# Kernel optimization log

Hardware: AMD Instinct MI355X
Metric: run time of the kernel (lower is better)

The kernel has to match this reference:

```python
import jax, jax.numpy as jnp
import numpy as np

N_SIGMA = 2
N_CLASS = 8
FG_WEIGHT = jnp.array([10., 10., 10., 40., 80., 100., 60., 20.], dtype=jnp.float32)
W_INST, W_VAR, W_SEED = 1.0, 10.0, 1.0
MIN_PIXELS = 128


def lovasz_hinge_flat(logits, labels):
    # logits, labels: [P] flat; labels in {0,1}
    signs = 2.0 * labels - 1.0
    errors = 1.0 - logits * signs
    order = jnp.argsort(-errors)  # descending
    errors_sorted = errors[order]
    gt_sorted = labels[order]
    gts = gt_sorted.sum()
    inter = gts - jnp.cumsum(gt_sorted)
    union = gts + jnp.cumsum(1.0 - gt_sorted)
    jac = 1.0 - inter / union
    grad = jnp.concatenate([jac[:1], jac[1:] - jac[:-1]])
    return jnp.dot(jax.nn.relu(errors_sorted), jax.lax.stop_gradient(grad))


def setup_inputs() -> dict:
    key = jax.random.key(0)
    k1, k2, k3, k4 = jax.random.split(key, 4)
    B, H, W, N = 2, 512, 1024, 8
    prediction = jax.random.normal(k1, (B, 12, H, W), dtype=jnp.float32)
    bbox = jax.random.randint(k2, (B, 9, H, W), 0, 2, dtype=jnp.int32)
    masks = jax.random.randint(k3, (B, N, H, W), 0, 2, dtype=jnp.int32)
    cls_ids = jax.random.randint(k4, (B, N), 0, 8, dtype=jnp.int32)
    return {"prediction": prediction, "bbox": bbox, "masks": masks, "cls_ids": cls_ids}


def _forward(prediction, bbox, masks, cls_ids):
    B, C, H, W = prediction.shape
    N = masks.shape[1]
    sg = jax.lax.stop_gradient
    # coordinate map: full 2048/1024 linspace sliced to [:W]/[:H], as in the buffer
    xm = jnp.linspace(0.0, 2.0, 2048, dtype=prediction.dtype)[:W]
    ym = jnp.linspace(0.0, 1.0, 1024, dtype=prediction.dtype)[:H]
    xym = jnp.stack([jnp.broadcast_to(xm[None, :], (H, W)),
                     jnp.broadcast_to(ym[:, None], (H, W))], axis=0)  # [2,H,W]

    spatial_emb = jnp.tanh(prediction[:, 0:2]) + xym[None]            # [B,2,H,W]
    sigma = prediction[:, 2:2 + N_SIGMA]                               # [B,2,H,W]
    seed = jax.nn.sigmoid(prediction[:, 2 + N_SIGMA:2 + N_SIGMA + N_CLASS])  # [B,8,H,W]

    # background seed loss: sum over cls 1..8 of seed[cls-1]^2 where bbox[cls]==0
    bg = bbox[:, 1:9] == 0                                             # [B,8,H,W]
    seed_bg = jnp.sum(jnp.where(bg, seed * seed, 0.0), axis=(1, 2, 3))  # [B]

    m = (masks > 0).astype(prediction.dtype)                           # [B,N,H,W]
    cnt = m.sum(axis=(2, 3))                                           # [B,N]
    valid = (cnt >= MIN_PIXELS).astype(prediction.dtype)               # [B,N]
    cnt_safe = jnp.maximum(cnt, 1.0)

    # per-instance masked means (to_center=False -> center from spatial_emb)
    center = jnp.einsum('bnhw,bchw->bnc', m, spatial_emb) / cnt_safe[..., None]  # [B,N,2]
    s_mean = jnp.einsum('bnhw,bchw->bnc', m, sigma) / cnt_safe[..., None]        # [B,N,2]

    # var loss: mean over [n_sigma, P] of (sigma_in - s.detach())^2
    diff2 = (sigma[:, None] - sg(s_mean)[..., None, None]) ** 2        # [B,N,2,H,W]
    var_inst = jnp.einsum('bnchw,bnhw->bn', diff2, m) / (N_SIGMA * cnt_safe)

    s_exp = jnp.exp(s_mean * 10.0)                                     # [B,N,2]
    d2 = (spatial_emb[:, None] - center[..., None, None]) ** 2         # [B,N,2,H,W]
    dist = jnp.exp(-jnp.einsum('bnchw,bnc->bnhw', d2, s_exp))          # [B,N,H,W]

    # lovasz hinge per instance on dist*2-1 vs mask
    logits = (dist * 2.0 - 1.0).reshape(B * N, H * W)
    labels = m.reshape(B * N, H * W)
    lov = jax.vmap(lovasz_hinge_flat)(logits, labels).reshape(B, N)    # [B,N]

    # foreground seed loss
    seed_cls = jnp.take_along_axis(seed, cls_ids[..., None, None].astype(jnp.int32), axis=1)  # [B,N,H,W]
    fw = FG_WEIGHT[cls_ids]                                            # [B,N]
    seed_fg = fw * jnp.einsum('bnhw,bnhw->bn', m, (seed_cls - sg(dist)) ** 2)

    obj = valid.sum(axis=1)                                            # [B]
    obj_safe = jnp.maximum(obj, 1.0)
    inst_l = jnp.sum(lov * valid, axis=1) / obj_safe
    var_l = jnp.sum(var_inst * valid, axis=1) / obj_safe
    seed_l = (seed_bg + jnp.sum(seed_fg * valid, axis=1)) / (H * W)
    loss = jnp.mean(W_INST * inst_l + W_VAR * var_l + W_SEED * seed_l)
    return loss


def reference(prediction, bbox, masks, cls_ids):
    return _forward(prediction, bbox, masks, cls_ids)
```

## Files before the change

### kernel.cpp

```cpp
#include <hip/hip_runtime.h>
#include <cstdint>
#include <cstddef>

#define HW 524288
#define HW4 131072
#define NBIN 1024


__device__ __forceinline__ float wred(float v) {
#pragma unroll
  for (int o = 32; o > 0; o >>= 1) v += __shfl_xor(v, o, 64);
  return v;
}

__device__ __forceinline__ float fsig(float x) {
  return __builtin_amdgcn_rcpf(1.f + __expf(-x));
}
__device__ __forceinline__ float ftanh(float x) {
  return 1.f - 2.f * __builtin_amdgcn_rcpf(__expf(2.f * x) + 1.f);
}

__global__ __launch_bounds__(256) void pass1(
    const float* __restrict__ pred, const int* __restrict__ masks,
    double* __restrict__ acc)
{
  const int b = blockIdx.y;
  const int tid = threadIdx.x;
  const float4* pb4 = (const float4*)(pred + (size_t)b * 12 * HW);
  const int4*   mk4 = (const int4*)(masks + (size_t)b * 8 * HW);

  float c[8] = {0}, cx[8] = {0}, cy[8] = {0}, sx[8] = {0}, sy[8] = {0},
        sxx[8] = {0}, syy[8] = {0};

#pragma unroll
  for (int k = 0; k < 2; k++) {
    const int g = blockIdx.x * 512 + k * 256 + tid;
    int idx = g << 2;
    int h = idx >> 10, w = idx & 1023;
    float4 p0 = pb4[g];
    float4 p1 = pb4[HW4 + g];
    float4 s0 = pb4[2 * HW4 + g];
    float4 s1 = pb4[3 * HW4 + g];
    int4 mv[8];
#pragma unroll
    for (int n = 0; n < 8; n++) mv[n] = mk4[n * HW4 + g];

    float p0v[4] = {p0.x, p0.y, p0.z, p0.w}, p1v[4] = {p1.x, p1.y, p1.z, p1.w};
    float s0v[4] = {s0.x, s0.y, s0.z, s0.w}, s1v[4] = {s1.x, s1.y, s1.z, s1.w};
    float exv[4], eyv[4];
#pragma unroll
    for (int j = 0; j < 4; j++) {
      exv[j] = ftanh(p0v[j]) + (float)((w + j) * (2.0 / 2047.0));
      eyv[j] = ftanh(p1v[j]) + (float)(h * (1.0 / 1023.0));
    }
#pragma unroll
    for (int n = 0; n < 8; n++) {
      int mvv[4] = {mv[n].x, mv[n].y, mv[n].z, mv[n].w};
#pragma unroll
      for (int j = 0; j < 4; j++) {
        float mf = (mvv[j] > 0) ? 1.f : 0.f;
        c[n] += mf; cx[n] += mf * exv[j]; cy[n] += mf * eyv[j];
        sx[n] += mf * s0v[j]; sy[n] += mf * s1v[j];
        sxx[n] += mf * s0v[j] * s0v[j]; syy[n] += mf * s1v[j] * s1v[j];
      }
    }
  }

  __shared__ float red[4][56];
  int lane = tid & 63, wid = tid >> 6;
#pragma unroll
  for (int n = 0; n < 8; n++) {
    float r0 = wred(c[n]),  r1 = wred(cx[n]), r2 = wred(cy[n]),
          r3 = wred(sx[n]), r4 = wred(sy[n]), r5 = wred(sxx[n]),
          r6 = wred(syy[n]);
    if (lane == 0) {
      red[wid][n * 7 + 0] = r0; red[wid][n * 7 + 1] = r1;
      red[wid][n * 7 + 2] = r2; red[wid][n * 7 + 3] = r3;
      red[wid][n * 7 + 4] = r4; red[wid][n * 7 + 5] = r5;
      red[wid][n * 7 + 6] = r6;
    }
  }
  __syncthreads();
  if (tid < 56) {
    float s = red[0][tid] + red[1][tid] + red[2][tid] + red[3][tid];
    int n = tid / 7, q = tid % 7;
    atomicAdd(&acc[((size_t)b * 8 + n) * 8 + q], (double)s);
  }
}

__global__ __launch_bounds__(1024) void pass3(
    const float* __restrict__ pred, const int* __restrict__ bbox,
    const int* __restrict__ masks, const int* __restrict__ cls_ids,
    double* __restrict__ acc, double* __restrict__ seedbg,
    unsigned long long* __restrict__ ghist)
{
  const int seg = blockIdx.y;
  const int b = seg >> 3, n = seg & 7;
  const int tid = threadIdx.x;
  __shared__ unsigned hist[NBIN];
  __shared__ float redf[16][2];
  for (int j = tid; j < NBIN; j += 1024) hist[j] = 0;

  const double* a = acc + seg * 8;
  double cntd = a[0];
  double cs = cntd < 1.0 ? 1.0 : cntd;
  float cxv = (float)(a[1] / cs), cyv = (float)(a[2] / cs);
  float sex = __expf((float)(a[3] / cs) * 10.f);
  float sey = __expf((float)(a[4] / cs) * 10.f);
  int cls = cls_ids[b * 8 + n];
  const float4* pb4 = (const float4*)(pred + (size_t)b * 12 * HW);
  const float4* sp4 = pb4 + (size_t)(4 + cls) * HW4;
  const float4* sb4 = pb4 + (size_t)(4 + n) * HW4;
  const int4*   mp4 = (const int4*)(masks + (size_t)seg * HW);
  const int4*   bb4 = (const int4*)(bbox + (size_t)b * 9 * HW) + (1 + n) * HW4;
  __syncthreads();

  float sf = 0.f, sbg = 0.f;
  int gbase = blockIdx.x * 4096;
#pragma unroll
  for (int i = 0; i < 4; i++) {
    int g = gbase + i * 1024 + tid;
    int idx = g << 2;
    int h = idx >> 10, w = idx & 1023;
    float4 p0 = pb4[g];
    float4 p1 = pb4[HW4 + g];
    int4 mv = mp4[g];
    float4 sv = sp4[g];
    float4 sb = sb4[g];
    int4 bv = bb4[g];
    float p0v[4] = {p0.x, p0.y, p0.z, p0.w}, p1v[4] = {p1.x, p1.y, p1.z, p1.w};
    float svv[4] = {sv.x, sv.y, sv.z, sv.w}, sbv[4] = {sb.x, sb.y, sb.z, sb.w};
    int mvv[4] = {mv.x, mv.y, mv.z, mv.w}, bvv[4] = {bv.x, bv.y, bv.z, bv.w};
#pragma unroll
    for (int j = 0; j < 4; j++) {
      int m = (mvv[j] > 0) ? 1 : 0;
      float ex = ftanh(p0v[j]) + (float)((w + j) * (2.0 / 2047.0));
      float ey = ftanh(p1v[j]) + (float)(h * (1.0 / 1023.0));
      float dx = ex - cxv, dy = ey - cyv;
      float d = __expf(-(dx * dx * sex + dy * dy * sey));
      float df = fsig(svv[j]) - d;
      sf += m ? df * df : 0.f;
      float sgb = fsig(sbv[j]);
      sbg += (bvv[j] == 0) ? sgb * sgb : 0.f;
      float e = m ? 2.f - 2.f * d : 2.f * d;
      int k = (int)(e * 512.f); k = k > (NBIN - 1) ? (NBIN - 1) : k;
      atomicAdd(&hist[k], m ? 65536u : 1u);
    }
  }
  __syncthreads();

  unsigned long long* gh = ghist + (size_t)seg * NBIN;
  for (int j = tid; j < NBIN; j += 1024) {
    unsigned v = hist[j];
    if (v)
      atomicAdd(&gh[j], (unsigned long long)(v & 0xffffu) |
                        ((unsigned long long)(v >> 16) << 32));
  }

  float r0 = wred(sf), r1 = wred(sbg);
  int lane = tid & 63, wid = tid >> 6;
  if (lane == 0) { redf[wid][0] = r0; redf[wid][1] = r1; }
  __syncthreads();
  if (tid == 0) {
    float t = 0.f;
    for (int w2 = 0; w2 < 16; w2++) t += redf[w2][0];
    atomicAdd(&acc[seg * 8 + 7], (double)t);
  } else if (tid == 64) {
    float t = 0.f;
    for (int w2 = 0; w2 < 16; w2++) t += redf[w2][1];
    atomicAdd(&seedbg[b], (double)t);
  }
}

__global__ __launch_bounds__(256) void pass4(
    const unsigned long long* __restrict__ ghist, const double* __restrict__ acc,
    const double* __restrict__ seedbg, const int* __restrict__ cls_ids,
    float* __restrict__ lov, unsigned* __restrict__ ctr,
    float* __restrict__ out)
{
  const int seg = blockIdx.x;
  const int tid = threadIdx.x;
  const int lane = tid & 63, wid = tid >> 6;
  __shared__ __align__(16) unsigned lh[NBIN * 2];
  __shared__ unsigned wc[4], wp[4];
  __shared__ double sred[4];

  const uint4* gh4 = (const uint4*)(ghist + (size_t)seg * NBIN);
#pragma unroll
  for (int i = 0; i < 2; i++)
    ((uint4*)lh)[i * 256 + tid] = gh4[i * 256 + tid];
  __syncthreads();

  double G = acc[seg * 8 + 0];

  unsigned cntT = 0, posT = 0;
#pragma unroll
  for (int i = 0; i < 4; i++) {
    int kk = (NBIN - 1) - tid * 4 - i;
    unsigned h0 = lh[2 * kk], h1 = lh[2 * kk + 1];
    cntT += h0 + h1; posT += h1;
  }
  unsigned ic = cntT, ip = posT;
  for (int o = 1; o < 64; o <<= 1) {
    unsigned yc = __shfl_up(ic, o, 64), yp = __shfl_up(ip, o, 64);
    if (lane >= o) { ic += yc; ip += yp; }
  }
  if (lane == 63) { wc[wid] = ic; wp[wid] = ip; }
  __syncthreads();
  unsigned oc = 0, op = 0;
  for (int w2 = 0; w2 < wid; w2++) { oc += wc[w2]; op += wp[w2]; }
  unsigned p = oc + ic - cntT, C = op + ip - posT;

  double S = 0.0;
#pragma unroll
  for (int i = 0; i < 4; i++) {
    int kk = (NBIN - 1) - tid * 4 - i;
    unsigned n1 = lh[2 * kk + 1], n0 = lh[2 * kk];
    double ec = (kk + 0.5) * (1.0 / 512.0);
    if (n1) {
      S += (double)n1 * ec / (G + (double)(p - C));
      p += n1; C += n1;
    }
    if (n0) {
      double rem = G - (double)C;
      if (rem > 0.0) {
        double aa = G + (double)(p - C);
        S += ec * rem * (1.0 / aa - 1.0 / (aa + (double)n0));
      }
      p += n0;
    }
  }
#pragma unroll
  for (int o = 32; o > 0; o >>= 1) S += __shfl_xor(S, o, 64);
  if (lane == 0) sred[wid] = S;
  __syncthreads();

  if (tid == 0) {
    double St = sred[0] + sred[1] + sred[2] + sred[3];
    atomicExch(&lov[seg], (float)St);
    __threadfence();
    unsigned old = atomicAdd(ctr, 1u);
    if (old == 15u) {
      __threadfence();
      const float FG[8] = {10.f, 10.f, 10.f, 40.f, 80.f, 100.f, 60.f, 20.f};
      double total = 0.0;
      for (int b = 0; b < 2; b++) {
        double obj = 0, inst = 0, varl = 0, sfg = 0;
        for (int n = 0; n < 8; n++) {
          int s = b * 8 + n;
          const double* a = acc + s * 8;
          double cnt = a[0];
          double cs = cnt < 1.0 ? 1.0 : cnt;
          double smx = a[3] / cs, smy = a[4] / cs;
          double var = ((a[5] - cnt * smx * smx) + (a[6] - cnt * smy * smy)) /
                       (2.0 * cs);
          double v = (cnt >= 128.0) ? 1.0 : 0.0;
          double lv = (double)atomicAdd(&lov[s], 0.0f);
          obj += v;
          inst += lv * v;
          varl += var * v;
          sfg += (double)FG[cls_ids[s]] * a[7] * v;
        }
        double objs = obj < 1.0 ? 1.0 : obj;
        double seedl = (seedbg[b] + sfg) / (double)HW;
        total += inst / objs + 10.0 * (varl / objs) + seedl;
      }
      out[0] = (float)(0.5 * total);
    }
  }
}

extern "C" void kernel_launch(void* const* d_in, const int* in_sizes, int n_in,
                              void* d_out, int out_size, void* d_ws, size_t ws_size,
                              hipStream_t stream)
{
  (void)in_sizes; (void)n_in; (void)out_size; (void)ws_size;
  const float* pred  = (const float*)d_in[0];
  const int*   bbox  = (const int*)d_in[1];
  const int*   masks = (const int*)d_in[2];
  const int*   cls   = (const int*)d_in[3];

  char* ws = (char*)d_ws;
  double*             acc    = (double*)(ws + 0);
  double*             seedbg = (double*)(ws + 1024);
  float*              lov    = (float*)(ws + 1040);
  unsigned*           ctr    = (unsigned*)(ws + 1104);
  unsigned long long* ghist  = (unsigned long long*)(ws + 4096);

  hipMemsetAsync(d_ws, 0, 135168, stream);
  pass1<<<dim3(256, 2), 256, 0, stream>>>(pred, masks, acc);
  pass3<<<dim3(32, 16), 1024, 0, stream>>>(pred, bbox, masks, cls, acc, seedbg, ghist);
  pass4<<<16, 256, 0, stream>>>(ghist, acc, seedbg, cls, lov, ctr, (float*)d_out);
}
```

Measured before the change: 170.9 us.

## Process all 8 instances per pixel block and dump per-block histograms

New measurement: 182.2 us. 1.07x slower.

```diff
diff --git a/kernel.cpp b/kernel.cpp
--- a/kernel.cpp
+++ b/kernel.cpp
@@ -88,87 +88,123 @@
   }
 }
 
-__global__ __launch_bounds__(1024) void pass3(
+__global__ __launch_bounds__(512) void pass3(
     const float* __restrict__ pred, const int* __restrict__ bbox,
     const int* __restrict__ masks, const int* __restrict__ cls_ids,
     double* __restrict__ acc, double* __restrict__ seedbg,
-    unsigned long long* __restrict__ ghist)
-{
-  const int seg = blockIdx.y;
+    unsigned* __restrict__ gdump)
+{
+  const int b = blockIdx.y;
+  const int tid = threadIdx.x;
+  __shared__ unsigned hist[8 * NBIN];
+  __shared__ float redf[8][9];
+
+  uint4* h4 = (uint4*)hist;
+  for (int j = tid; j < 2048; j += 512) h4[j] = make_uint4(0u, 0u, 0u, 0u);
+
+  float cxp[8], cyp[8], sexp[8], seyp[8];
+  int clsv[8];
+#pragma unroll
+  for (int n = 0; n < 8; n++) {
+    const double* a = acc + ((size_t)b * 8 + n) * 8;
+    double cs = a[0] < 1.0 ? 1.0 : a[0];
+    cxp[n] = (float)(a[1] / cs);
+    cyp[n] = (float)(a[2] / cs);
+    sexp[n] = __expf((float)(a[3] / cs) * 10.f);
+    seyp[n] = __expf((float)(a[4] / cs) * 10.f);
+    clsv[n] = cls_ids[b * 8 + n];
+  }
+  const float4* pb4 = (const float4*)(pred + (size_t)b * 12 * HW);
+  const int4*   mk4 = (const int4*)(masks + (size_t)b * 8 * HW);
+  const int4*   bb4 = (const int4*)(bbox + (size_t)b * 9 * HW);
+  __syncthreads();
+
+  const int g = blockIdx.x * 512 + tid;
+  const int idx = g << 2;
+  const int h = idx >> 10, w = idx & 1023;
+
+  float4 p0 = pb4[g];
+  float4 p1 = pb4[HW4 + g];
+  float ex[4], ey[4];
+  {
+    float p0v[4] = {p0.x, p0.y, p0.z, p0.w}, p1v[4] = {p1.x, p1.y, p1.z, p1.w};
+#pragma unroll
+    for (int j = 0; j < 4; j++) {
+      ex[j] = ftanh(p0v[j]) + (float)((w + j) * (2.0 / 2047.0));
+      ey[j] = ftanh(p1v[j]) + (float)(h * (1.0 / 1023.0));
+    }
+  }
+
+  float sbg = 0.f;
+  int lane = tid & 63, wid = tid >> 6;
+#pragma unroll
+  for (int n = 0; n < 8; n++) {
+    int4   mv = mk4[n * HW4 + g];
+    int4   bv = bb4[(1 + n) * HW4 + g];
+    float4 sc = pb4[(4 + clsv[n]) * HW4 + g];
+    float4 sb = pb4[(4 + n) * HW4 + g];
+    int mvv[4] = {mv.x, mv.y, mv.z, mv.w}, bvv[4] = {bv.x, bv.y, bv.z, bv.w};
+    float scv[4] = {sc.x, sc.y, sc.z, sc.w}, sbv[4] = {sb.x, sb.y, sb.z, sb.w};
+    float sf = 0.f;
+#pragma unroll
+    for (int j = 0; j < 4; j++) {
+      int m = (mvv[j] > 0) ? 1 : 0;
+      float dx = ex[j] - cxp[n], dy = ey[j] - cyp[n];
+      float d = __expf(-(dx * dx * sexp[n] + dy * dy * seyp[n]));
+      float df = fsig(scv[j]) - d;
+      sf += m ? df * df : 0.f;
+      float s0 = fsig(sbv[j]);
+      sbg += (bvv[j] == 0) ? s0 * s0 : 0.f;
+      float e = m ? 2.f - 2.f * d : 2.f * d;
+      int k = (int)(e * 512.f); k = k > (NBIN - 1) ? (NBIN - 1) : k;
+      atomicAdd(&hist[n * NBIN + k], m ? 65536u : 1u);
+    }
+    float r = wred(sf);
+    if (lane == 0) redf[wid][n] = r;
+  }
+  {
+    float r = wred(sbg);
+    if (lane == 0) redf[wid][8] = r;
+  }
+  __syncthreads();
+
+  uint4* dst = (uint4*)(gdump + ((size_t)(b * 256 + blockIdx.x) * 8) * NBIN);
+  for (int j = tid; j < 2048; j += 512) dst[j] = h4[j];
+
+  if (tid < 9) {
+    float t = 0.f;
+    for (int w2 = 0; w2 < 8; w2++) t += redf[w2][tid];
+    if (tid < 8)
+      atomicAdd(&acc[((size_t)b * 8 + tid) * 8 + 7], (double)t);
+    else
+      atomicAdd(&seedbg[b], (double)t);
+  }
+}
+
+__global__ __launch_bounds__(256) void pass4a(
+    const unsigned* __restrict__ gdump, unsigned long long* __restrict__ ghist)
+{
+  const int seg = blockIdx.x >> 4;
+  const int chunk = blockIdx.x & 15;
   const int b = seg >> 3, n = seg & 7;
   const int tid = threadIdx.x;
-  __shared__ unsigned hist[NBIN];
-  __shared__ float redf[16][2];
-  for (int j = tid; j < NBIN; j += 1024) hist[j] = 0;
-
-  const double* a = acc + seg * 8;
-  double cntd = a[0];
-  double cs = cntd < 1.0 ? 1.0 : cntd;
-  float cxv = (float)(a[1] / cs), cyv = (float)(a[2] / cs);
-  float sex = __expf((float)(a[3] / cs) * 10.f);
-  float sey = __expf((float)(a[4] / cs) * 10.f);
-  int cls = cls_ids[b * 8 + n];
-  const float4* pb4 = (const float4*)(pred + (size_t)b * 12 * HW);
-  const float4* sp4 = pb4 + (size_t)(4 + cls) * HW4;
-  const float4* sb4 = pb4 + (size_t)(4 + n) * HW4;
-  const int4*   mp4 = (const int4*)(masks + (size_t)seg * HW);
-  const int4*   bb4 = (const int4*)(bbox + (size_t)b * 9 * HW) + (1 + n) * HW4;
-  __syncthreads();
-
-  float sf = 0.f, sbg = 0.f;
-  int gbase = blockIdx.x * 4096;
+
+  unsigned neg[4] = {0, 0, 0, 0}, pos[4] = {0, 0, 0, 0};
+#pragma unroll
+  for (int xb = 0; xb < 16; xb++) {
+    int blk = chunk * 16 + xb;
+    const uint4 v = ((const uint4*)gdump)[(((size_t)b * 256 + blk) * 8 + n) * 256 + tid];
+    neg[0] += v.x & 0xffffu; pos[0] += v.x >> 16;
+    neg[1] += v.y & 0xffffu; pos[1] += v.y >> 16;
+    neg[2] += v.z & 0xffffu; pos[2] += v.z >> 16;
+    neg[3] += v.w & 0xffffu; pos[3] += v.w >> 16;
+  }
+  unsigned long long* gh = ghist + (size_t)seg * NBIN;
 #pragma unroll
   for (int i = 0; i < 4; i++) {
-    int g = gbase + i * 1024 + tid;
-    int idx = g << 2;
-    int h = idx >> 10, w = idx & 1023;
-    float4 p0 = pb4[g];
-    float4 p1 = pb4[HW4 + g];
-    int4 mv = mp4[g];
-    float4 sv = sp4[g];
-    float4 sb = sb4[g];
-    int4 bv = bb4[g];
-    float p0v[4] = {p0.x, p0.y, p0.z, p0.w}, p1v[4] = {p1.x, p1.y, p1.z, p1.w};
-    float svv[4] = {sv.x, sv.y, sv.z, sv.w}, sbv[4] = {sb.x, sb.y, sb.z, sb.w};
-    int mvv[4] = {mv.x, mv.y, mv.z, mv.w}, bvv[4] = {bv.x, bv.y, bv.z, bv.w};
-#pragma unroll
-    for (int j = 0; j < 4; j++) {
-      int m = (mvv[j] > 0) ? 1 : 0;
-      float ex = ftanh(p0v[j]) + (float)((w + j) * (2.0 / 2047.0));
-      float ey = ftanh(p1v[j]) + (float)(h * (1.0 / 1023.0));
-      float dx = ex - cxv, dy = ey - cyv;
-      float d = __expf(-(dx * dx * sex + dy * dy * sey));
-      float df = fsig(svv[j]) - d;
-      sf += m ? df * df : 0.f;
-      float sgb = fsig(sbv[j]);
-      sbg += (bvv[j] == 0) ? sgb * sgb : 0.f;
-      float e = m ? 2.f - 2.f * d : 2.f * d;
-      int k = (int)(e * 512.f); k = k > (NBIN - 1) ? (NBIN - 1) : k;
-      atomicAdd(&hist[k], m ? 65536u : 1u);
-    }
-  }
-  __syncthreads();
-
-  unsigned long long* gh = ghist + (size_t)seg * NBIN;
-  for (int j = tid; j < NBIN; j += 1024) {
-    unsigned v = hist[j];
-    if (v)
-      atomicAdd(&gh[j], (unsigned long long)(v & 0xffffu) |
-                        ((unsigned long long)(v >> 16) << 32));
-  }
-
-  float r0 = wred(sf), r1 = wred(sbg);
-  int lane = tid & 63, wid = tid >> 6;
-  if (lane == 0) { redf[wid][0] = r0; redf[wid][1] = r1; }
-  __syncthreads();
-  if (tid == 0) {
-    float t = 0.f;
-    for (int w2 = 0; w2 < 16; w2++) t += redf[w2][0];
-    atomicAdd(&acc[seg * 8 + 7], (double)t);
-  } else if (tid == 64) {
-    float t = 0.f;
-    for (int w2 = 0; w2 < 16; w2++) t += redf[w2][1];
-    atomicAdd(&seedbg[b], (double)t);
+    if (neg[i] | pos[i])
+      atomicAdd(&gh[tid * 4 + i],
+                (unsigned long long)neg[i] | ((unsigned long long)pos[i] << 32));
   }
 }
 
@@ -286,9 +322,11 @@
   float*              lov    = (float*)(ws + 1040);
   unsigned*           ctr    = (unsigned*)(ws + 1104);
   unsigned long long* ghist  = (unsigned long long*)(ws + 4096);
+  unsigned*           gdump  = (unsigned*)(ws + 262144);
 
   hipMemsetAsync(d_ws, 0, 135168, stream);
   pass1<<<dim3(256, 2), 256, 0, stream>>>(pred, masks, acc);
-  pass3<<<dim3(32, 16), 1024, 0, stream>>>(pred, bbox, masks, cls, acc, seedbg, ghist);
+  pass3<<<dim3(256, 2), 512, 0, stream>>>(pred, bbox, masks, cls, acc, seedbg, gdump);
+  pass4a<<<256, 256, 0, stream>>>(gdump, ghist);
   pass4<<<16, 256, 0, stream>>>(ghist, acc, seedbg, cls, lov, ctr, (float*)d_out);
 }
```

## Fuse Lovasz histogram scan into pass3 via last-block counter, split pass1 wider

Applied to the files above, without the earlier changes.

New measurement: 298.1 us. 74.4% more time.

```diff
diff --git a/kernel.cpp b/kernel.cpp
--- a/kernel.cpp
+++ b/kernel.cpp
@@ -12,7 +12,6 @@
   for (int o = 32; o > 0; o >>= 1) v += __shfl_xor(v, o, 64);
   return v;
 }
-
 __device__ __forceinline__ float fsig(float x) {
   return __builtin_amdgcn_rcpf(1.f + __expf(-x));
 }
@@ -29,40 +28,39 @@
   const float4* pb4 = (const float4*)(pred + (size_t)b * 12 * HW);
   const int4*   mk4 = (const int4*)(masks + (size_t)b * 8 * HW);
 
-  float c[8] = {0}, cx[8] = {0}, cy[8] = {0}, sx[8] = {0}, sy[8] = {0},
-        sxx[8] = {0}, syy[8] = {0};
-
-#pragma unroll
-  for (int k = 0; k < 2; k++) {
-    const int g = blockIdx.x * 512 + k * 256 + tid;
-    int idx = g << 2;
-    int h = idx >> 10, w = idx & 1023;
-    float4 p0 = pb4[g];
-    float4 p1 = pb4[HW4 + g];
-    float4 s0 = pb4[2 * HW4 + g];
-    float4 s1 = pb4[3 * HW4 + g];
-    int4 mv[8];
-#pragma unroll
-    for (int n = 0; n < 8; n++) mv[n] = mk4[n * HW4 + g];
-
-    float p0v[4] = {p0.x, p0.y, p0.z, p0.w}, p1v[4] = {p1.x, p1.y, p1.z, p1.w};
-    float s0v[4] = {s0.x, s0.y, s0.z, s0.w}, s1v[4] = {s1.x, s1.y, s1.z, s1.w};
-    float exv[4], eyv[4];
+  const int g = blockIdx.x * 256 + tid;
+  const int idx = g << 2;
+  const int h = idx >> 10, w = idx & 1023;
+
+  float4 p0 = pb4[g];
+  float4 p1 = pb4[HW4 + g];
+  float4 s0 = pb4[2 * HW4 + g];
+  float4 s1 = pb4[3 * HW4 + g];
+  int4 mv[8];
+#pragma unroll
+  for (int n = 0; n < 8; n++) mv[n] = mk4[n * HW4 + g];
+
+  float p0v[4] = {p0.x, p0.y, p0.z, p0.w}, p1v[4] = {p1.x, p1.y, p1.z, p1.w};
+  float s0v[4] = {s0.x, s0.y, s0.z, s0.w}, s1v[4] = {s1.x, s1.y, s1.z, s1.w};
+  float exv[4], eyv[4];
+#pragma unroll
+  for (int j = 0; j < 4; j++) {
+    exv[j] = ftanh(p0v[j]) + (float)((w + j) * (2.0 / 2047.0));
+    eyv[j] = ftanh(p1v[j]) + (float)(h * (1.0 / 1023.0));
+  }
+
+  float c[8], cx[8], cy[8], sx[8], sy[8], sxx[8], syy[8];
+#pragma unroll
+  for (int n = 0; n < 8; n++) {
+    c[n] = 0.f; cx[n] = 0.f; cy[n] = 0.f; sx[n] = 0.f; sy[n] = 0.f;
+    sxx[n] = 0.f; syy[n] = 0.f;
+    int mvv[4] = {mv[n].x, mv[n].y, mv[n].z, mv[n].w};
 #pragma unroll
     for (int j = 0; j < 4; j++) {
-      exv[j] = ftanh(p0v[j]) + (float)((w + j) * (2.0 / 2047.0));
-      eyv[j] = ftanh(p1v[j]) + (float)(h * (1.0 / 1023.0));
-    }
-#pragma unroll
-    for (int n = 0; n < 8; n++) {
-      int mvv[4] = {mv[n].x, mv[n].y, mv[n].z, mv[n].w};
-#pragma unroll
-      for (int j = 0; j < 4; j++) {
-        float mf = (mvv[j] > 0) ? 1.f : 0.f;
-        c[n] += mf; cx[n] += mf * exv[j]; cy[n] += mf * eyv[j];
-        sx[n] += mf * s0v[j]; sy[n] += mf * s1v[j];
-        sxx[n] += mf * s0v[j] * s0v[j]; syy[n] += mf * s1v[j] * s1v[j];
-      }
+      float mf = (mvv[j] > 0) ? 1.f : 0.f;
+      c[n] += mf; cx[n] += mf * exv[j]; cy[n] += mf * eyv[j];
+      sx[n] += mf * s0v[j]; sy[n] += mf * s1v[j];
+      sxx[n] += mf * s0v[j] * s0v[j]; syy[n] += mf * s1v[j] * s1v[j];
     }
   }
 
@@ -88,17 +86,25 @@
   }
 }
 
-__global__ __launch_bounds__(1024) void pass3(
+__global__ __launch_bounds__(1024) void pass3g(
     const float* __restrict__ pred, const int* __restrict__ bbox,
     const int* __restrict__ masks, const int* __restrict__ cls_ids,
     double* __restrict__ acc, double* __restrict__ seedbg,
-    unsigned long long* __restrict__ ghist)
+    unsigned long long* __restrict__ ghist, float* __restrict__ lov,
+    unsigned* __restrict__ ctr3, unsigned* __restrict__ ctr2,
+    float* __restrict__ out)
 {
   const int seg = blockIdx.y;
   const int b = seg >> 3, n = seg & 7;
   const int tid = threadIdx.x;
-  __shared__ unsigned hist[NBIN];
+  const int lane = tid & 63, wid = tid >> 6;
+  __shared__ __align__(16) unsigned smem[2 * NBIN];
   __shared__ float redf[16][2];
+  __shared__ unsigned wc[4], wp[4];
+  __shared__ double sred[4];
+  __shared__ unsigned oldsh;
+
+  unsigned* hist = smem;
   for (int j = tid; j < NBIN; j += 1024) hist[j] = 0;
 
   const double* a = acc + seg * 8;
@@ -156,10 +162,10 @@
       atomicAdd(&gh[j], (unsigned long long)(v & 0xffffu) |
                         ((unsigned long long)(v >> 16) << 32));
   }
-
-  float r0 = wred(sf), r1 = wred(sbg);
-  int lane = tid & 63, wid = tid >> 6;
-  if (lane == 0) { redf[wid][0] = r0; redf[wid][1] = r1; }
+  {
+    float r0 = wred(sf), r1 = wred(sbg);
+    if (lane == 0) { redf[wid][0] = r0; redf[wid][1] = r1; }
+  }
   __syncthreads();
   if (tid == 0) {
     float t = 0.f;
@@ -170,99 +176,103 @@
     for (int w2 = 0; w2 < 16; w2++) t += redf[w2][1];
     atomicAdd(&seedbg[b], (double)t);
   }
-}
-
-__global__ __launch_bounds__(256) void pass4(
-    const unsigned long long* __restrict__ ghist, const double* __restrict__ acc,
-    const double* __restrict__ seedbg, const int* __restrict__ cls_ids,
-    float* __restrict__ lov, unsigned* __restrict__ ctr,
-    float* __restrict__ out)
-{
-  const int seg = blockIdx.x;
-  const int tid = threadIdx.x;
-  const int lane = tid & 63, wid = tid >> 6;
-  __shared__ __align__(16) unsigned lh[NBIN * 2];
-  __shared__ unsigned wc[4], wp[4];
-  __shared__ double sred[4];
-
-  const uint4* gh4 = (const uint4*)(ghist + (size_t)seg * NBIN);
-#pragma unroll
-  for (int i = 0; i < 2; i++)
-    ((uint4*)lh)[i * 256 + tid] = gh4[i * 256 + tid];
-  __syncthreads();
-
-  double G = acc[seg * 8 + 0];
-
-  unsigned cntT = 0, posT = 0;
-#pragma unroll
-  for (int i = 0; i < 4; i++) {
-    int kk = (NBIN - 1) - tid * 4 - i;
-    unsigned h0 = lh[2 * kk], h1 = lh[2 * kk + 1];
-    cntT += h0 + h1; posT += h1;
-  }
-  unsigned ic = cntT, ip = posT;
-  for (int o = 1; o < 64; o <<= 1) {
-    unsigned yc = __shfl_up(ic, o, 64), yp = __shfl_up(ip, o, 64);
-    if (lane >= o) { ic += yc; ip += yp; }
-  }
-  if (lane == 63) { wc[wid] = ic; wp[wid] = ip; }
-  __syncthreads();
-  unsigned oc = 0, op = 0;
-  for (int w2 = 0; w2 < wid; w2++) { oc += wc[w2]; op += wp[w2]; }
-  unsigned p = oc + ic - cntT, C = op + ip - posT;
-
-  double S = 0.0;
-#pragma unroll
-  for (int i = 0; i < 4; i++) {
-    int kk = (NBIN - 1) - tid * 4 - i;
-    unsigned n1 = lh[2 * kk + 1], n0 = lh[2 * kk];
-    double ec = (kk + 0.5) * (1.0 / 512.0);
-    if (n1) {
-      S += (double)n1 * ec / (G + (double)(p - C));
-      p += n1; C += n1;
-    }
-    if (n0) {
-      double rem = G - (double)C;
-      if (rem > 0.0) {
-        double aa = G + (double)(p - C);
-        S += ec * rem * (1.0 / aa - 1.0 / (aa + (double)n0));
+
+  __threadfence();
+  __syncthreads();
+  if (tid == 0) oldsh = atomicAdd(&ctr3[seg], 1u);
+  __syncthreads();
+  if (oldsh != 31u) return;
+
+  unsigned* lh = smem;
+  if (tid < 256) {
+#pragma unroll
+    for (int i = 0; i < 4; i++) {
+      unsigned long long v = atomicAdd(&gh[tid * 4 + i], 0ULL);
+      lh[2 * (tid * 4 + i)]     = (unsigned)(v & 0xffffffffULL);
+      lh[2 * (tid * 4 + i) + 1] = (unsigned)(v >> 32);
+    }
+  }
+  __syncthreads();
+
+  double G = cntd;
+
+  unsigned p = 0, C = 0, cntT = 0, posT = 0;
+  if (tid < 256) {
+#pragma unroll
+    for (int i = 0; i < 4; i++) {
+      int kk = (NBIN - 1) - tid * 4 - i;
+      unsigned h0 = lh[2 * kk], h1 = lh[2 * kk + 1];
+      cntT += h0 + h1; posT += h1;
+    }
+    unsigned ic = cntT, ip = posT;
+    for (int o = 1; o < 64; o <<= 1) {
+      unsigned yc = __shfl_up(ic, o, 64), yp = __shfl_up(ip, o, 64);
+      if (lane >= o) { ic += yc; ip += yp; }
+    }
+    if (lane == 63) { wc[wid] = ic; wp[wid] = ip; }
+    p = ic; C = ip;
+  }
+  __syncthreads();
+  if (tid < 256) {
+    unsigned oc = 0, op = 0;
+    for (int w2 = 0; w2 < wid; w2++) { oc += wc[w2]; op += wp[w2]; }
+    p = oc + p - cntT; C = op + C - posT;
+
+    double S = 0.0;
+#pragma unroll
+    for (int i = 0; i < 4; i++) {
+      int kk = (NBIN - 1) - tid * 4 - i;
+      unsigned n1 = lh[2 * kk + 1], n0 = lh[2 * kk];
+      double ec = (kk + 0.5) * (1.0 / 512.0);
+      if (n1) {
+        S += (double)n1 * ec / (G + (double)(p - C));
+        p += n1; C += n1;
       }
-      p += n0;
-    }
-  }
-#pragma unroll
-  for (int o = 32; o > 0; o >>= 1) S += __shfl_xor(S, o, 64);
-  if (lane == 0) sred[wid] = S;
+      if (n0) {
+        double rem = G - (double)C;
+        if (rem > 0.0) {
+          double aa = G + (double)(p - C);
+          S += ec * rem * (1.0 / aa - 1.0 / (aa + (double)n0));
+        }
+        p += n0;
+      }
+    }
+#pragma unroll
+    for (int o = 32; o > 0; o >>= 1) S += __shfl_xor(S, o, 64);
+    if (lane == 0) sred[wid] = S;
+  }
   __syncthreads();
 
   if (tid == 0) {
     double St = sred[0] + sred[1] + sred[2] + sred[3];
     atomicExch(&lov[seg], (float)St);
     __threadfence();
-    unsigned old = atomicAdd(ctr, 1u);
-    if (old == 15u) {
+    unsigned old2 = atomicAdd(ctr2, 1u);
+    if (old2 == 15u) {
       __threadfence();
       const float FG[8] = {10.f, 10.f, 10.f, 40.f, 80.f, 100.f, 60.f, 20.f};
       double total = 0.0;
-      for (int b = 0; b < 2; b++) {
+      for (int bb = 0; bb < 2; bb++) {
         double obj = 0, inst = 0, varl = 0, sfg = 0;
-        for (int n = 0; n < 8; n++) {
-          int s = b * 8 + n;
-          const double* a = acc + s * 8;
-          double cnt = a[0];
-          double cs = cnt < 1.0 ? 1.0 : cnt;
-          double smx = a[3] / cs, smy = a[4] / cs;
-          double var = ((a[5] - cnt * smx * smx) + (a[6] - cnt * smy * smy)) /
-                       (2.0 * cs);
+        for (int nn = 0; nn < 8; nn++) {
+          int s = bb * 8 + nn;
+          const double* a2 = acc + s * 8;
+          double cnt = a2[0];
+          double cs2 = cnt < 1.0 ? 1.0 : cnt;
+          double smx = a2[3] / cs2, smy = a2[4] / cs2;
+          double var = ((a2[5] - cnt * smx * smx) + (a2[6] - cnt * smy * smy)) /
+                       (2.0 * cs2);
           double v = (cnt >= 128.0) ? 1.0 : 0.0;
+          double sfv = atomicAdd(&acc[s * 8 + 7], 0.0);
           double lv = (double)atomicAdd(&lov[s], 0.0f);
           obj += v;
           inst += lv * v;
           varl += var * v;
-          sfg += (double)FG[cls_ids[s]] * a[7] * v;
+          sfg += (double)FG[cls_ids[s]] * sfv * v;
         }
         double objs = obj < 1.0 ? 1.0 : obj;
-        double seedl = (seedbg[b] + sfg) / (double)HW;
+        double sbgv = atomicAdd(&seedbg[bb], 0.0);
+        double seedl = (sbgv + sfg) / (double)HW;
         total += inst / objs + 10.0 * (varl / objs) + seedl;
       }
       out[0] = (float)(0.5 * total);
@@ -284,11 +294,12 @@
   double*             acc    = (double*)(ws + 0);
   double*             seedbg = (double*)(ws + 1024);
   float*              lov    = (float*)(ws + 1040);
-  unsigned*           ctr    = (unsigned*)(ws + 1104);
+  unsigned*           ctr3   = (unsigned*)(ws + 1104);
+  unsigned*           ctr2   = (unsigned*)(ws + 1168);
   unsigned long long* ghist  = (unsigned long long*)(ws + 4096);
 
   hipMemsetAsync(d_ws, 0, 135168, stream);
-  pass1<<<dim3(256, 2), 256, 0, stream>>>(pred, masks, acc);
-  pass3<<<dim3(32, 16), 1024, 0, stream>>>(pred, bbox, masks, cls, acc, seedbg, ghist);
-  pass4<<<16, 256, 0, stream>>>(ghist, acc, seedbg, cls, lov, ctr, (float*)d_out);
-}
+  pass1<<<dim3(512, 2), 256, 0, stream>>>(pred, masks, acc);
+  pass3g<<<dim3(32, 16), 1024, 0, stream>>>(pred, bbox, masks, cls, acc, seedbg,
+                                            ghist, lov, ctr3, ctr2, (float*)d_out);
+}
```
